# Kernel optimization log

Hardware: AMD Instinct MI355X
Metric: run time of the kernel (lower is better)

The kernel has to match this reference:

```python
import jax, jax.numpy as jnp
import numpy as np

B = 1; NCAM = 6; DM = 256; NH = 8; HD = 32; NL = 4; NP = 4; NZ = 2
BEV_H = 100; BEV_W = 100; NQ = BEV_H * BEV_W
IMG_H = 450; IMG_W = 800
SHAPES = [(56, 100), (28, 50), (14, 25), (7, 13)]
Z_CANDI = [0.0, 2.0]
H_METERS = 100.0; W_METERS = 100.0; OFFSET = 0.0
DFF = 1024


def _grid3d():
    # generate_grid + V_inv projection + z-anchor stacking (GenerateGrid)
    xs = (np.arange(BEV_W) + 0.5) / BEV_W
    ys = (np.arange(BEV_H) + 0.5) / BEV_H
    X, Y = np.meshgrid(xs, ys, indexing='xy')
    g = np.stack([X * BEV_W, Y * BEV_H, np.ones_like(X)], 0).reshape(3, -1)
    sh = BEV_H / H_METERS; sw = BEV_W / W_METERS
    V = np.array([[0., -sw, BEV_W / 2.], [-sh, 0., BEV_H * OFFSET + BEV_H / 2.], [0., 0., 1.]])
    g = np.linalg.inv(V) @ g  # (3, NQ), meters
    g3 = np.stack([np.concatenate([g[:2], np.full((1, g.shape[1]), z)], 0) for z in Z_CANDI], 0)
    return jnp.asarray(g3, jnp.float32)  # (NZ, 3, NQ)


def _ref2d():
    x = np.linspace(0, 1, BEV_W); y = np.linspace(0, 1, BEV_H)
    X, Y = np.meshgrid(x, y, indexing='xy')
    return jnp.asarray(np.stack([X, Y], -1).reshape(1, NQ, 2), jnp.float32)


def _pos_emb():
    # PositionEmbeddingSine(num_pos_feats=128, normalize=True)
    nf = DM // 2; scale = 2 * np.pi; eps = 1e-6
    y = (np.arange(1, BEV_H + 1, dtype=np.float64) - 0.5) / (BEV_H + eps) * scale
    x = (np.arange(1, BEV_W + 1, dtype=np.float64) - 0.5) / (BEV_W + eps) * scale
    dim_t = 10000.0 ** (2 * (np.arange(nf) // 2) / nf)
    def emb(v):
        p = v[:, None] / dim_t
        return np.stack([np.sin(p[:, 0::2]), np.cos(p[:, 1::2])], -1).reshape(v.shape[0], nf)
    ey = emb(y); ex = emb(x)
    pos = np.concatenate([np.broadcast_to(ey[:, None, :], (BEV_H, BEV_W, nf)),
                          np.broadcast_to(ex[None, :, :], (BEV_H, BEV_W, nf))], -1)
    return jnp.asarray(pos.reshape(1, NQ, DM), jnp.float32)


def _project(I, E):
    # ReferencePoints.get_3d
    g = _grid3d()
    g = jnp.concatenate([g, jnp.ones((NZ, 1, NQ), jnp.float32)], 1)  # (NZ,4,NQ) homo
    cam = jnp.einsum('bnij,djl->bndil', E, g)               # (B,N,NZ,4,NQ)
    img = jnp.einsum('bnij,bndjl->bndil', I, cam[:, :, :, :3])  # (B,N,NZ,3,NQ)
    eps = 1e-5
    z = img[:, :, :, 2:3]
    pts = img[:, :, :, :2] / jnp.maximum(z, eps)
    m = (z > eps) & (pts[:, :, :, 0:1] > 0) & (pts[:, :, :, 0:1] < IMG_W) \
        & (pts[:, :, :, 1:2] > 0) & (pts[:, :, :, 1:2] < IMG_H)
    pts = pts / jnp.array([IMG_W, IMG_H], jnp.float32)[None, None, None, :, None]
    ref = pts.transpose(0, 1, 4, 2, 3)                       # (B,N,NQ,NZ,2)
    mask = jnp.broadcast_to(m, (B, NCAM, NZ, 2, NQ)).transpose(0, 1, 4, 2, 3)
    return ref, mask


def _ln(x, g, b):
    mu = x.mean(-1, keepdims=True)
    var = ((x - mu) ** 2).mean(-1, keepdims=True)
    return (x - mu) * jax.lax.rsqrt(var + 1e-5) * g + b


def _bilinear(value, loc, H, W):
    # grid_sample, bilinear, zero padding, align_corners=False
    # value: (BB, H*W, C); loc: (BB, Q, 2) normalized (x,y) in [0,1]
    x = loc[..., 0] * W - 0.5
    y = loc[..., 1] * H - 0.5
    x0 = jnp.floor(x); y0 = jnp.floor(y)
    wx = (x - x0)[..., None]; wy = (y - y0)[..., None]
    x0 = x0.astype(jnp.int32); y0 = y0.astype(jnp.int32)
    def g(xi, yi):
        ok = ((xi >= 0) & (xi < W) & (yi >= 0) & (yi < H))[..., None]
        idx = jnp.clip(yi, 0, H - 1) * W + jnp.clip(xi, 0, W - 1)
        return jnp.take_along_axis(value, idx[..., None], axis=1) * ok
    return (g(x0, y0) * (1 - wx) * (1 - wy) + g(x0 + 1, y0) * wx * (1 - wy)
            + g(x0, y0 + 1) * (1 - wx) * wy + g(x0 + 1, y0 + 1) * wx * wy)


def _forward(queries_prev, features_0, features_1, features_2, features_3, intrinsics, extrinsic,
             bev_q_init, level_embed, cams_embed,
             ws_off, bs_off, ws_attn, bs_attn, ws_val, bs_val, ws_out, bs_out, g1, be1,
             wc_off, bc_off, wc_attn, bc_attn, wc_val, bc_val, wc_out, bc_out, g2, be2,
             w1, b1, w2, b2, g3, be3):
    feats = [features_0, features_1, features_2, features_3]
    queries = bev_q_init[None] + queries_prev  # (B,NQ,DM)
    ref3d, bmask = _project(intrinsics, extrinsic)
    ref2d = _ref2d(); pos = _pos_emb()
    # ---- deformable self-attention over the BEV grid (single level) ----
    q = queries + pos
    off = (q @ ws_off + bs_off).reshape(B, NQ, NH, NP, 2)
    aw = jax.nn.softmax((q @ ws_attn + bs_attn).reshape(B, NQ, NH, NP), -1)
    val = (queries @ ws_val + bs_val).reshape(B, NQ, NH, HD).transpose(0, 2, 1, 3).reshape(B * NH, NQ, HD)
    loc = ref2d[:, :, None, None, :] + off / jnp.array([BEV_W, BEV_H], jnp.float32)
    loc = loc.transpose(0, 2, 1, 3, 4).reshape(B * NH, NQ * NP, 2)
    s = _bilinear(val, loc, BEV_H, BEV_W).reshape(B, NH, NQ, NP, HD)
    sa = jnp.einsum('bhqpe,bqhp->bqhe', s, aw).reshape(B, NQ, DM) @ ws_out + bs_out
    queries = _ln(queries + sa, g1, be1)
    # ---- multi-camera multi-scale deformable cross-attention ----
    q = queries + pos
    offc = (q @ wc_off + bc_off).reshape(B, NQ, NH, NL, NZ, NP, 2)
    awc = jax.nn.softmax((q @ wc_attn + bc_attn).reshape(B, NQ, NH, NL * NZ * NP), -1)
    awc = awc.reshape(B, NQ, NH, NL, NZ, NP)
    acc = jnp.zeros((B, NCAM, NQ, NH, HD), queries.dtype)
    for l in range(NL):
        Hl, Wl = SHAPES[l]
        f = feats[l].reshape(B, NCAM, DM, Hl * Wl).transpose(0, 1, 3, 2)
        f = f + level_embed[l] + cams_embed[None, :, None, :]
        v = (f @ wc_val + bc_val).reshape(B, NCAM, Hl * Wl, NH, HD)
        v = v.transpose(0, 1, 3, 2, 4).reshape(B * NCAM * NH, Hl * Wl, HD)
        loc = ref3d[:, :, :, None, :, None, :] + (offc[:, None, :, :, l] / jnp.array([Wl, Hl], jnp.float32))
        loc = loc.transpose(0, 1, 3, 2, 4, 5, 6).reshape(B * NCAM * NH, NQ * NZ * NP, 2)
        s = _bilinear(v, loc, Hl, Wl).reshape(B, NCAM, NH, NQ, NZ, NP, HD)
        acc = acc + jnp.einsum('bnhqzpe,bqhzp->bnqhe', s, awc[:, :, :, l])
    out = acc.reshape(B, NCAM, NQ, DM) @ wc_out + bc_out
    valid = jnp.any(bmask[..., 0], axis=-1).astype(queries.dtype)  # (B,NCAM,NQ)
    cnt = jnp.maximum(valid.sum(1), 1.0)
    ca = (out * valid[..., None]).sum(1) / cnt[..., None]
    queries = _ln(queries + ca, g2, be2)
    # ---- FFN ----
    h = jax.nn.relu(queries @ w1 + b1) @ w2 + b2
    queries = _ln(queries + h, g3, be3)
    return queries


def setup_inputs() -> dict:
    key = jax.random.key(0)
    ks = jax.random.split(key, 24)
    def w(k, shape, s=0.02):
        return jax.random.normal(k, shape, jnp.float32) * s
    inp = {}
    inp['queries_prev'] = w(ks[0], (B, NQ, DM), 1.0)
    for i, (Hl, Wl) in enumerate(SHAPES):
        inp['features_' + str(i)] = w(ks[1 + i], (B * NCAM, DM, Hl, Wl), 1.0)
    I = np.zeros((B, NCAM, 3, 3), np.float32)
    I[..., 0, 0] = 400.0; I[..., 1, 1] = 400.0
    I[..., 0, 2] = IMG_W / 2.0; I[..., 1, 2] = IMG_H / 2.0; I[..., 2, 2] = 1.0
    Es = []
    for i in range(NCAM):
        th = 2 * np.pi * i / NCAM
        fwd = np.array([np.cos(th), np.sin(th), 0.0])
        rgt = np.array([np.sin(th), -np.cos(th), 0.0])
        dwn = np.array([0.0, 0.0, -1.0])
        R = np.stack([rgt, dwn, fwd], 0)
        t = -R @ (1.0 * fwd + np.array([0.0, 0.0, 1.5]))
        E = np.eye(4, dtype=np.float32); E[:3, :3] = R; E[:3, 3] = t
        Es.append(E)
    inp['intrinsics'] = jnp.asarray(I)
    inp['extrinsic'] = jnp.asarray(np.stack(Es).astype(np.float32)[None])
    inp['bev_q_init'] = w(ks[5], (NQ, DM))
    inp['level_embed'] = w(ks[6], (NL, DM))
    inp['cams_embed'] = w(ks[7], (NCAM, DM))
    inp['ws_off'] = w(ks[8], (DM, NH * NP * 2)); inp['bs_off'] = jnp.zeros((NH * NP * 2,), jnp.float32)
    inp['ws_attn'] = w(ks[9], (DM, NH * NP)); inp['bs_attn'] = jnp.zeros((NH * NP,), jnp.float32)
    inp['ws_val'] = w(ks[10], (DM, DM)); inp['bs_val'] = jnp.zeros((DM,), jnp.float32)
    inp['ws_out'] = w(ks[11], (DM, DM)); inp['bs_out'] = jnp.zeros((DM,), jnp.float32)
    inp['g1'] = jnp.ones((DM,), jnp.float32); inp['be1'] = jnp.zeros((DM,), jnp.float32)
    inp['wc_off'] = w(ks[12], (DM, NH * NL * NZ * NP * 2)); inp['bc_off'] = jnp.zeros((NH * NL * NZ * NP * 2,), jnp.float32)
    inp['wc_attn'] = w(ks[13], (DM, NH * NL * NZ * NP)); inp['bc_attn'] = jnp.zeros((NH * NL * NZ * NP,), jnp.float32)
    inp['wc_val'] = w(ks[14], (DM, DM)); inp['bc_val'] = jnp.zeros((DM,), jnp.float32)
    inp['wc_out'] = w(ks[15], (DM, DM)); inp['bc_out'] = jnp.zeros((DM,), jnp.float32)
    inp['g2'] = jnp.ones((DM,), jnp.float32); inp['be2'] = jnp.zeros((DM,), jnp.float32)
    inp['w1'] = w(ks[16], (DM, DFF)); inp['b1'] = jnp.zeros((DFF,), jnp.float32)
    inp['w2'] = w(ks[17], (DFF, DM)); inp['b2'] = jnp.zeros((DM,), jnp.float32)
    inp['g3'] = jnp.ones((DM,), jnp.float32); inp['be3'] = jnp.zeros((DM,), jnp.float32)
    return inp


def reference(queries_prev, features_0, features_1, features_2, features_3, intrinsics, extrinsic,
              bev_q_init, level_embed, cams_embed,
              ws_off, bs_off, ws_attn, bs_attn, ws_val, bs_val, ws_out, bs_out, g1, be1,
              wc_off, bc_off, wc_attn, bc_attn, wc_val, bc_val, wc_out, bc_out, g2, be2,
              w1, b1, w2, b2, g3, be3):
    return _forward(queries_prev, features_0, features_1, features_2, features_3, intrinsics, extrinsic,
                    bev_q_init, level_embed, cams_embed,
                    ws_off, bs_off, ws_attn, bs_attn, ws_val, bs_val, ws_out, bs_out, g1, be1,
                    wc_off, bc_off, wc_attn, bc_attn, wc_val, bc_val, wc_out, bc_out, g2, be2,
                    w1, b1, w2, b2, g3, be3)
```

## Files before the change

kernel.cpp:

```cpp
#include <hip/hip_runtime.h>
#include <hip/hip_bf16.h>
#include <math.h>

typedef __hip_bfloat16 bf16;
typedef __attribute__((ext_vector_type(8))) short short8;
typedef __attribute__((ext_vector_type(4))) float f32x4;
typedef __attribute__((ext_vector_type(2))) float f32x2;

__device__ __forceinline__ float b2f(bf16 v) { return __bfloat162float(v); }
__device__ __forceinline__ unsigned short f2bf(float f) {
    bf16 h = __float2bfloat16(f);
    return *(unsigned short*)&h;
}
__device__ __forceinline__ float bflo(unsigned u) { return __uint_as_float(u << 16); }
__device__ __forceinline__ float bfhi(unsigned u) { return __uint_as_float(u & 0xFFFF0000u); }
__device__ __forceinline__ f32x2 bf2(unsigned u) {
    f32x2 r;
    r.x = __uint_as_float(u << 16);
    r.y = __uint_as_float(u & 0xFFFF0000u);
    return r;
}

__device__ __forceinline__ float ldin(const void* p, size_t i, int isbf) {
    return isbf ? b2f(((const bf16*)p)[i]) : ((const float*)p)[i];
}

__global__ void detect_kernel(const unsigned* __restrict__ g1raw, int* __restrict__ flag)
{
    if (threadIdx.x == 0 && blockIdx.x == 0)
        flag[0] = (g1raw[0] == 0x3F803F80u) ? 1 : 0;
}

struct WTArg { const void* src[10]; int K[10]; int N[10]; int dstoff[10]; int cumt[11]; };
__global__ __launch_bounds__(256) void convert_wt_kernel(WTArg a, const int* __restrict__ flagp,
                                                         bf16* __restrict__ dst)
{
    __shared__ float T[64][65];
    int b = blockIdx.x, t = threadIdx.x;
    int isbf = flagp[0];
    int i = 0;
    while (b >= a.cumt[i + 1]) i++;
    int r = b - a.cumt[i];
    int K = a.K[i], N = a.N[i];
    int ntn = (N + 63) >> 6;
    int tk = r / ntn, tn = r - tk * ntn;
    int k0 = tk * 64, n0 = tn * 64;
    int nn = t & 63, kr = t >> 6;
#pragma unroll
    for (int ii = 0; ii < 16; ii++) {
        int k = kr + ii * 4;
        float v = 0.f;
        if (n0 + nn < N) v = ldin(a.src[i], (size_t)(k0 + k) * N + n0 + nn, isbf);
        T[k][nn] = v;
    }
    __syncthreads();
    int k2 = (t & 31) * 2, nr = t >> 5;
#pragma unroll
    for (int ii = 0; ii < 8; ii++) {
        int n = nr + ii * 8;
        if (n0 + n < N) {
            unsigned lo = f2bf(T[k2][n]);
            unsigned hi = f2bf(T[k2 + 1][n]);
            *(unsigned*)&dst[a.dstoff[i] + (size_t)(n0 + n) * K + k0 + k2] = lo | (hi << 16);
        }
    }
}

struct VConvArg { const void* src[16]; int cum[17]; };
__global__ __launch_bounds__(256) void convert_v_kernel(VConvArg a, const int* __restrict__ flagp,
                                                        float* __restrict__ dst)
{
    int g = blockIdx.x * 256 + threadIdx.x;
    if (g >= a.cum[16]) return;
    int isbf = flagp[0];
    int i = 0;
    while (g >= a.cum[i + 1]) i++;
    dst[g] = ldin(a.src[i], g - a.cum[i], isbf);
}

__global__ __launch_bounds__(256) void ptable_kernel(float* __restrict__ ptab)
{
    int idx = blockIdx.x * 256 + threadIdx.x;
    if (idx >= 12800) return;
    int a = idx >> 7, dd = idx & 127;
    float v = ((float)a + 0.5f) * (6.2831853071795864f / 100.000001f);
    float e = (float)(dd & ~1) * (1.f / 128.f);
    float freq = expf(e * 9.210340371976184f);
    float tt = v / freq;
    ptab[idx] = (dd & 1) ? cosf(tt) : sinf(tt);
}

#define KSTR 72
template<int BM>
__global__ __launch_bounds__(256) void mfma_gemm_t(
    const bf16* __restrict__ A, const bf16* __restrict__ Wt,
    const float* __restrict__ bias, float* __restrict__ C, bf16* __restrict__ Cbf,
    int M, int N, int K, int act)
{
    constexpr int MT = BM / 32;
    __shared__ unsigned short As[BM * KSTR];
    __shared__ unsigned short Ws[64 * KSTR];
    const int t = threadIdx.x;
    const int wave = t >> 6, lane = t & 63;
    const int qd = lane >> 4, l15 = lane & 15;
    const int m0 = blockIdx.x * BM, n0 = blockIdx.y * 64;
    const int wm = (wave >> 1) * (BM / 2), wn = (wave & 1) * 32;

    f32x4 acc[MT][2] = {};

    const int r_a = t >> 3, c8_a = t & 7;
    const int r_w = t >> 3, c8_w = t & 7;

    for (int k0 = 0; k0 < K; k0 += 64) {
        uint4 va[MT], vw[2];
#pragma unroll
        for (int i = 0; i < MT; i++)
            va[i] = *(const uint4*)(A + (size_t)(m0 + r_a + i * 32) * K + k0 + c8_a * 8);
#pragma unroll
        for (int i = 0; i < 2; i++)
            vw[i] = *(const uint4*)(Wt + (size_t)(n0 + r_w + i * 32) * K + k0 + c8_w * 8);
#pragma unroll
        for (int i = 0; i < MT; i++)
            *(uint4*)&As[(r_a + i * 32) * KSTR + c8_a * 8] = va[i];
#pragma unroll
        for (int i = 0; i < 2; i++)
            *(uint4*)&Ws[(r_w + i * 32) * KSTR + c8_w * 8] = vw[i];
        __syncthreads();
#pragma unroll
        for (int kk = 0; kk < 2; kk++) {
            short8 af[MT], bfr[2];
#pragma unroll
            for (int mi = 0; mi < MT; mi++)
                af[mi] = *(const short8*)&As[(wm + mi * 16 + l15) * KSTR + kk * 32 + qd * 8];
#pragma unroll
            for (int ni = 0; ni < 2; ni++)
                bfr[ni] = *(const short8*)&Ws[(wn + ni * 16 + l15) * KSTR + kk * 32 + qd * 8];
#pragma unroll
            for (int mi = 0; mi < MT; mi++)
#pragma unroll
                for (int ni = 0; ni < 2; ni++)
                    acc[mi][ni] = __builtin_amdgcn_mfma_f32_16x16x32_bf16(af[mi], bfr[ni], acc[mi][ni], 0, 0, 0);
        }
        __syncthreads();
    }
#pragma unroll
    for (int mi = 0; mi < MT; mi++) {
#pragma unroll
        for (int ni = 0; ni < 2; ni++) {
            int col = n0 + wn + ni * 16 + l15;
            if (col >= N) continue;
            float bv = bias ? bias[col] : 0.f;
#pragma unroll
            for (int r = 0; r < 4; r++) {
                int rowm = m0 + wm + mi * 16 + qd * 4 + r;
                if (rowm >= M) continue;
                float v = acc[mi][ni][r] + bv;
                if (act == 1) v = fmaxf(v, 0.f);
                if (Cbf) Cbf[(size_t)rowm * N + col] = __float2bfloat16(v);
                else     C[(size_t)rowm * N + col] = v;
            }
        }
    }
}

__global__ __launch_bounds__(256) void init_kernel(
    const void* __restrict__ qprev, const void* __restrict__ qinit, const int* __restrict__ flagp,
    const float* __restrict__ ptab,
    float* __restrict__ queries, bf16* __restrict__ queries_bf, bf16* __restrict__ qbuf_bf)
{
    int qi = blockIdx.x, d = threadIdx.x;
    int isbf = flagp[0];
    size_t idx = (size_t)qi * 256 + d;
    float qv = ldin(qinit, idx, isbf) + ldin(qprev, idx, isbf);
    int row = qi / 100, col = qi % 100;
    float pv = (d < 128) ? ptab[row * 128 + d] : ptab[col * 128 + (d - 128)];
    queries[idx] = qv;
    queries_bf[idx] = __float2bfloat16(qv);
    qbuf_bf[idx] = __float2bfloat16(qv + pv);
}

__global__ __launch_bounds__(256) void proj_kernel(
    const void* __restrict__ intr, const void* __restrict__ extr, const int* __restrict__ flagp,
    float* __restrict__ ref3d, float* __restrict__ valid)
{
    int idx = blockIdx.x * 256 + threadIdx.x;
    if (idx >= 60000) return;
    int isbf = flagp[0];
    int cam = idx / 10000, qi = idx % 10000;
    int row = qi / 100, col = qi % 100;
    float X = 49.5f - (float)row, Y = 49.5f - (float)col;
    float E[12];
#pragma unroll
    for (int i = 0; i < 12; i++) E[i] = ldin(extr, cam * 16 + i, isbf);
    float I9[9];
#pragma unroll
    for (int i = 0; i < 9; i++) I9[i] = ldin(intr, cam * 9 + i, isbf);
    bool any = false;
#pragma unroll
    for (int z = 0; z < 2; z++) {
        float Z = (z == 0) ? 0.f : 2.f;
        float c0 = E[0] * X + E[1] * Y + E[2] * Z + E[3];
        float c1 = E[4] * X + E[5] * Y + E[6] * Z + E[7];
        float c2 = E[8] * X + E[9] * Y + E[10] * Z + E[11];
        float i0 = I9[0] * c0 + I9[1] * c1 + I9[2] * c2;
        float i1 = I9[3] * c0 + I9[4] * c1 + I9[5] * c2;
        float i2 = I9[6] * c0 + I9[7] * c1 + I9[8] * c2;
        float zc = fmaxf(i2, 1e-5f);
        float px = i0 / zc, py = i1 / zc;
        bool m = (i2 > 1e-5f) && (px > 0.f) && (px < 800.f) && (py > 0.f) && (py < 450.f);
        any = any || m;
        ref3d[cam * 40000 + qi * 4 + z * 2 + 0] = px * (1.f / 800.f);
        ref3d[cam * 40000 + qi * 4 + z * 2 + 1] = py * (1.f / 450.f);
    }
    valid[cam * 10000 + qi] = any ? 1.f : 0.f;
}

__global__ __launch_bounds__(256) void tsa_sample_kernel(
    const float* __restrict__ ps, const float* __restrict__ val, bf16* __restrict__ sa_pre_bf)
{
    int blk = (blockIdx.x & 7) * 625 + (blockIdx.x >> 3);
    int qbase = blk * 2;
    int t = threadIdx.x;
    __shared__ float s_ps[192];
    __shared__ int4   s_tidx[64];
    __shared__ float4 s_tw[64];
    if (t < 192) s_ps[t] = ps[(size_t)qbase * 96 + t];
    __syncthreads();
    if (t < 64) {
        int q = t >> 5, r = t & 31, h = r >> 2, p = r & 3;
        int qi = qbase + q;
        const float* pq = s_ps + q * 96;
        float a0 = pq[64 + h * 4 + 0], a1 = pq[64 + h * 4 + 1];
        float a2 = pq[64 + h * 4 + 2], a3 = pq[64 + h * 4 + 3];
        float m = fmaxf(fmaxf(a0, a1), fmaxf(a2, a3));
        float den = expf(a0 - m) + expf(a1 - m) + expf(a2 - m) + expf(a3 - m);
        float aw = expf(pq[64 + h * 4 + p] - m) / den;
        float rx = (float)(qi % 100) * (1.f / 99.f);
        float ry = (float)(qi / 100) * (1.f / 99.f);
        float lx = rx + pq[h * 8 + p * 2 + 0] * 0.01f;
        float ly = ry + pq[h * 8 + p * 2 + 1] * 0.01f;
        float x = fminf(fmaxf(lx * 100.f - 0.5f, -2.0e6f), 2.0e6f);
        float y = fminf(fmaxf(ly * 100.f - 0.5f, -2.0e6f), 2.0e6f);
        float xf = floorf(x), yf = floorf(y);
        int x0 = (int)xf, y0 = (int)yf;
        float wx = x - xf, wy = y - yf;
        bool okx0 = (x0 >= 0) && (x0 < 100), okx1 = (x0 + 1 >= 0) && (x0 + 1 < 100);
        bool oky0 = (y0 >= 0) && (y0 < 100), oky1 = (y0 + 1 >= 0) && (y0 + 1 < 100);
        int x0c = min(max(x0, 0), 99), x1c = min(max(x0 + 1, 0), 99);
        int y0c = min(max(y0, 0), 99), y1c = min(max(y0 + 1, 0), 99);
        s_tidx[t] = make_int4((y0c * 100 + x0c) * 256, (y0c * 100 + x1c) * 256,
                              (y1c * 100 + x0c) * 256, (y1c * 100 + x1c) * 256);
        s_tw[t] = make_float4(aw * (1.f - wx) * (1.f - wy) * ((okx0 && oky0) ? 1.f : 0.f),
                              aw * wx * (1.f - wy) * ((okx1 && oky0) ? 1.f : 0.f),
                              aw * (1.f - wx) * wy * ((okx0 && oky1) ? 1.f : 0.f),
                              aw * wx * wy * ((okx1 && oky1) ? 1.f : 0.f));
    }
    __syncthreads();
    int q = t >> 7, c2 = t & 127, h = c2 >> 4;
    f32x2 V[4][4];
    float4 W[4];
#pragma unroll
    for (int p = 0; p < 4; p++) {
        int4 ix = s_tidx[q * 32 + h * 4 + p];
        W[p] = s_tw[q * 32 + h * 4 + p];
        V[p][0] = *(const f32x2*)(val + ix.x + 2 * c2);
        V[p][1] = *(const f32x2*)(val + ix.y + 2 * c2);
        V[p][2] = *(const f32x2*)(val + ix.z + 2 * c2);
        V[p][3] = *(const f32x2*)(val + ix.w + 2 * c2);
    }
    f32x2 acc = {0.f, 0.f};
#pragma unroll
    for (int p = 0; p < 4; p++)
        acc += V[p][0] * W[p].x + V[p][1] * W[p].y + V[p][2] * W[p].z + V[p][3] * W[p].w;
    int qi = qbase + q;
    unsigned lo = (unsigned)f2bf(acc.x) | ((unsigned)f2bf(acc.y) << 16);
    *(unsigned*)&sa_pre_bf[(size_t)qi * 256 + c2 * 2] = lo;
}

__global__ __launch_bounds__(256) void build_f_t_kernel(
    const void* __restrict__ f0, const void* __restrict__ f1,
    const void* __restrict__ f2, const void* __restrict__ f3,
    const void* __restrict__ lvl_emb, const void* __restrict__ cam_emb,
    const int* __restrict__ flagp, bf16* __restrict__ f_all)
{
    const int HWs[4]   = {5600, 1400, 350, 91};
    const int ptls[4]  = {88, 22, 6, 2};
    const int cumt[5]  = {0, 2112, 2640, 2784, 2832};
    const int rowb[4]  = {0, 33600, 42000, 44100};
    __shared__ float T[64][65];
    int b = blockIdx.x, t = threadIdx.x;
    int isbf = flagp[0];
    int l = 0;
    while (b >= cumt[l + 1]) l++;
    int r = b - cumt[l];
    int npt = ptls[l], HW = HWs[l];
    int cam = r / (4 * npt); r -= cam * 4 * npt;
    int dt = r / npt;
    int pt = r - dt * npt;
    const void* f = (l == 0) ? f0 : (l == 1) ? f1 : (l == 2) ? f2 : f3;

    int p = t & 63, dr = t >> 6;
    int pix = pt * 64 + p;
#pragma unroll
    for (int i = 0; i < 16; i++) {
        int d = dr + i * 4;
        float v = 0.f;
        if (pix < HW) v = ldin(f, (size_t)(cam * 256 + dt * 64 + d) * HW + pix, isbf);
        T[d][p] = v;
    }
    __syncthreads();
    int c2 = t & 31, pr0 = t >> 5;
    int dcol = dt * 64 + c2 * 2;
    float emb0 = ldin(lvl_emb, l * 256 + dcol, isbf) + ldin(cam_emb, cam * 256 + dcol, isbf);
    float emb1 = ldin(lvl_emb, l * 256 + dcol + 1, isbf) + ldin(cam_emb, cam * 256 + dcol + 1, isbf);
#pragma unroll
    for (int i = 0; i < 8; i++) {
        int px = pt * 64 + pr0 + i * 8;
        if (px < HW) {
            unsigned lo = f2bf(T[c2 * 2][pr0 + i * 8] + emb0);
            unsigned hi = f2bf(T[c2 * 2 + 1][pr0 + i * 8] + emb1);
            *(unsigned*)&f_all[(size_t)(rowb[l] + cam * HW + px) * 256 + dcol] = lo | (hi << 16);
        }
    }
}

__global__ __launch_bounds__(256) void cross_sample_kernel(
    const float* __restrict__ ref3d, const float* __restrict__ valid,
    const float* __restrict__ projc, const bf16* __restrict__ vall,
    bf16* __restrict__ ca_pre_bf, float* __restrict__ anyv)
{
    int qi = (blockIdx.x & 7) * 1250 + (blockIdx.x >> 3);
    int t = threadIdx.x;
    __shared__ float s_off[512];
    __shared__ float s_aw[256], s_ref[24], s_val[8];
    __shared__ int   s_cam[8];
    __shared__ int   s_nv;
    __shared__ int4   s_idx[512];
    __shared__ float4 s_w[512];
    const float* row = projc + (size_t)qi * 768;
    s_off[t]       = row[t];
    s_off[256 + t] = row[256 + t];
    float araw     = row[512 + t];
    if (t < 24) s_ref[t] = ref3d[(t >> 2) * 40000 + qi * 4 + (t & 3)];
    if (t >= 32 && t < 38) s_val[t - 32] = valid[(t - 32) * 10000 + qi];
    float m = araw;
#pragma unroll
    for (int mask = 16; mask >= 1; mask >>= 1) m = fmaxf(m, __shfl_xor(m, mask));
    float ev = expf(araw - m);
    float ssum = ev;
#pragma unroll
    for (int mask = 16; mask >= 1; mask >>= 1) ssum += __shfl_xor(ssum, mask);
    s_aw[t] = ev / ssum;
    __syncthreads();

    if (t == 0) {
        int n = 0;
#pragma unroll
        for (int c = 0; c < 6; c++)
            if (s_val[c] != 0.f) s_cam[n++] = c;
        s_nv = n;
    }
    __syncthreads();
    const int nv = s_nv;

    const int   Hs[4]    = {56, 28, 14, 7};
    const int   Wl[4]    = {100, 50, 25, 13};
    const int   HWs[4]   = {5600, 1400, 350, 91};
    const int   bases[4] = {0, 33600, 42000, 44100};
    const float invW[4]  = {1.f / 100.f, 1.f / 50.f, 1.f / 25.f, 1.f / 13.f};
    const float invH[4]  = {1.f / 56.f, 1.f / 28.f, 1.f / 14.f, 1.f / 7.f};

    const int c8 = t & 31, g = t >> 5, h = c8 >> 2;
    f32x2 q01 = {0.f, 0.f}, q23 = {0.f, 0.f}, q45 = {0.f, 0.f}, q67 = {0.f, 0.f};
    const unsigned short* vp = (const unsigned short*)vall;

    for (int cc0 = 0; cc0 < nv; cc0 += 2) {
#pragma unroll
        for (int cl = 0; cl < 2; cl++) {
            int e = t + cl * 256;
            if (cc0 + cl < nv) {
                int cam = s_cam[cc0 + cl];
                int rem = e & 255;
                int s = rem >> 3, hh = rem & 7;
                int l = s >> 3, z = (s >> 2) & 1;
                int W = Wl[l], H = Hs[l];
                float lx = s_ref[cam * 4 + z * 2 + 0] + s_off[hh * 64 + s * 2 + 0] * invW[l];
                float ly = s_ref[cam * 4 + z * 2 + 1] + s_off[hh * 64 + s * 2 + 1] * invH[l];
                float x = fminf(fmaxf(lx * (float)W - 0.5f, -2.0e6f), 2.0e6f);
                float y = fminf(fmaxf(ly * (float)H - 0.5f, -2.0e6f), 2.0e6f);
                float xf = floorf(x), yf = floorf(y);
                int x0 = (int)xf, y0 = (int)yf;
                float wx = x - xf, wy = y - yf;
                bool okx0 = (x0 >= 0) && (x0 < W);
                bool okx1 = (x0 + 1 >= 0) && (x0 + 1 < W);
                bool oky0 = (y0 >= 0) && (y0 < H);
                bool oky1 = (y0 + 1 >= 0) && (y0 + 1 < H);
                int x0c = min(max(x0, 0), W - 1), x1c = min(max(x0 + 1, 0), W - 1);
                int y0c = min(max(y0, 0), H - 1), y1c = min(max(y0 + 1, 0), H - 1);
                int base = (bases[l] + cam * HWs[l]) * 256;
                float awv = s_aw[hh * 32 + s];
                s_idx[e] = make_int4(base + (y0c * W + x0c) * 256,
                                     base + (y0c * W + x1c) * 256,
                                     base + (y1c * W + x0c) * 256,
                                     base + (y1c * W + x1c) * 256);
                s_w[e] = make_float4(awv * (1.f - wx) * (1.f - wy) * (okx0 && oky0 ? 1.f : 0.f),
                                     awv * wx * (1.f - wy) * (okx1 && oky0 ? 1.f : 0.f),
                                     awv * (1.f - wx) * wy * (okx0 && oky1 ? 1.f : 0.f),
                                     awv * wx * wy * (okx1 && oky1 ? 1.f : 0.f));
            }
        }
        __syncthreads();

#pragma unroll
        for (int cl = 0; cl < 2; cl++) {
            if (cc0 + cl < nv) {
                int eb = cl * 256 + g * 32 + h;
                int4   IX[4];
                float4 W[4];
                uint4  U[4][4];
#pragma unroll
                for (int j = 0; j < 4; j++) { IX[j] = s_idx[eb + j * 8]; W[j] = s_w[eb + j * 8]; }
#pragma unroll
                for (int j = 0; j < 4; j++) {
                    U[j][0] = *(const uint4*)(vp + IX[j].x + c8 * 8);
                    U[j][1] = *(const uint4*)(vp + IX[j].y + c8 * 8);
                    U[j][2] = *(const uint4*)(vp + IX[j].z + c8 * 8);
                    U[j][3] = *(const uint4*)(vp + IX[j].w + c8 * 8);
                }
#pragma unroll
                for (int j = 0; j < 4; j++) {
                    float4 w = W[j];
                    q01 += bf2(U[j][0].x) * w.x + bf2(U[j][1].x) * w.y + bf2(U[j][2].x) * w.z + bf2(U[j][3].x) * w.w;
                    q23 += bf2(U[j][0].y) * w.x + bf2(U[j][1].y) * w.y + bf2(U[j][2].y) * w.z + bf2(U[j][3].y) * w.w;
                    q45 += bf2(U[j][0].z) * w.x + bf2(U[j][1].z) * w.y + bf2(U[j][2].z) * w.z + bf2(U[j][3].z) * w.w;
                    q67 += bf2(U[j][0].w) * w.x + bf2(U[j][1].w) * w.y + bf2(U[j][2].w) * w.z + bf2(U[j][3].w) * w.w;
                }
            }
        }
        __syncthreads();
    }

    float inv_cnt = 1.f / fmaxf((float)nv, 1.f);
    float4* s_red = (float4*)s_idx;
    s_red[t]       = make_float4(q01.x, q01.y, q23.x, q23.y);
    s_red[256 + t] = make_float4(q45.x, q45.y, q67.x, q67.y);
    __syncthreads();
    if (t < 32) {
        float4 A = make_float4(0.f, 0.f, 0.f, 0.f), B = make_float4(0.f, 0.f, 0.f, 0.f);
#pragma unroll
        for (int gg = 0; gg < 8; gg++) {
            float4 a = s_red[gg * 32 + t], b = s_red[256 + gg * 32 + t];
            A.x += a.x; A.y += a.y; A.z += a.z; A.w += a.w;
            B.x += b.x; B.y += b.y; B.z += b.z; B.w += b.w;
        }
        unsigned w0 = (unsigned)f2bf(A.x * inv_cnt) | ((unsigned)f2bf(A.y * inv_cnt) << 16);
        unsigned w1 = (unsigned)f2bf(A.z * inv_cnt) | ((unsigned)f2bf(A.w * inv_cnt) << 16);
        unsigned w2 = (unsigned)f2bf(B.x * inv_cnt) | ((unsigned)f2bf(B.y * inv_cnt) << 16);
        unsigned w3 = (unsigned)f2bf(B.z * inv_cnt) | ((unsigned)f2bf(B.w * inv_cnt) << 16);
        *(uint4*)&ca_pre_bf[(size_t)qi * 256 + t * 8] = make_uint4(w0, w1, w2, w3);
    }
    if (t == 0) anyv[qi] = (nv > 0) ? 1.f : 0.f;
}

__global__ __launch_bounds__(256) void ln_kernel(
    float* __restrict__ queries, const float* __restrict__ x,
    const float* __restrict__ rowflag, const float* __restrict__ extra_bias,
    const float* __restrict__ g, const float* __restrict__ be,
    bf16* __restrict__ qpos_bf, bf16* __restrict__ nrm_bf, float* __restrict__ nrm_f32,
    const float* __restrict__ ptab)
{
    int qi = blockIdx.x, d = threadIdx.x;
    size_t idx = (size_t)qi * 256 + d;
    float r = queries[idx] + x[idx];
    if (extra_bias) r += rowflag[qi] * extra_bias[d];
    __shared__ float red1[4], red2[4];
    float s = r;
#pragma unroll
    for (int o = 32; o > 0; o >>= 1) s += __shfl_down(s, o, 64);
    if ((d & 63) == 0) red1[d >> 6] = s;
    __syncthreads();
    float mu = (red1[0] + red1[1] + red1[2] + red1[3]) * (1.f / 256.f);
    float dv = r - mu;
    float s2 = dv * dv;
#pragma unroll
    for (int o = 32; o > 0; o >>= 1) s2 += __shfl_down(s2, o, 64);
    if ((d & 63) == 0) red2[d >> 6] = s2;
    __syncthreads();
    float var = (red2[0] + red2[1] + red2[2] + red2[3]) * (1.f / 256.f);
    float nrm = dv * rsqrtf(var + 1e-5f) * g[d] + be[d];
    queries[idx] = nrm;
    if (qpos_bf) {
        int row = qi / 100, col = qi % 100;
        float pv = (d < 128) ? ptab[row * 128 + d] : ptab[col * 128 + (d - 128)];
        qpos_bf[idx] = __float2bfloat16(nrm + pv);
    }
    if (nrm_bf)  nrm_bf[idx]  = __float2bfloat16(nrm);
    if (nrm_f32) nrm_f32[idx] = nrm;
}

extern "C" void kernel_launch(void* const* d_in, const int* in_sizes, int n_in,
                              void* d_out, int out_size, void* d_ws, size_t ws_size,
                              hipStream_t stream)
{
    const void* qprev   = d_in[0];
    const void* f0      = d_in[1];
    const void* f1      = d_in[2];
    const void* f2      = d_in[3];
    const void* f3      = d_in[4];
    const void* intr    = d_in[5];
    const void* extr    = d_in[6];
    const void* qinit   = d_in[7];
    const void* lvl_emb = d_in[8];
    const void* cam_emb = d_in[9];

    float* ws = (float*)d_ws;
    float* queries    = ws + 0;
    float* ref3d      = ws + 2560000;
    float* valid      = ws + 2800000;
    float* anyv       = ws + 2860000;
    int*   flagp      = (int*)(ws + 2870000);
    float* biases     = ws + 2880000;
    bf16*  wconv_bf   = (bf16*)(ws + 2890000);
    bf16*  queries_bf = (bf16*)(ws + 3400000);
    bf16*  qbuf_bf    = (bf16*)(ws + 4680000);
    float* proj_s     = ws + 5960000;
    float* projc      = ws + 6920000;
    bf16*  vall_bf    = (bf16*)(ws + 14600000);
    float* RA         = ws + 20320000;
    float* val        = RA;
    bf16*  sa_pre_bf  = (bf16*)(RA + 2560000);
    float* sa         = RA + 3840000;
    bf16*  f_all_bf   = (bf16*)RA;
    bf16*  ca_pre_bf  = (bf16*)RA;
    float* ca         = RA + 1280000;
    bf16*  q2_bf      = (bf16*)(RA + 3840000);
    bf16*  hffn_bf    = (bf16*)(RA + 5120000);
    float* ffnout     = RA + 10240000;
    float* ptab       = ws + 33150000;

    if (ws_size < (size_t)33320000 * sizeof(float)) return;

    WTArg wa;
    {
        const int si[10] = {10, 12, 14, 16, 20, 22, 24, 26, 30, 32};
        const int Ks[10] = {256, 256, 256, 256, 256, 256, 256, 256, 256, 1024};
        const int Ns[10] = {64, 32, 256, 256, 512, 256, 256, 256, 1024, 256};
        int cum = 0, cumt = 0;
        for (int i = 0; i < 10; i++) {
            wa.src[i] = d_in[si[i]]; wa.K[i] = Ks[i]; wa.N[i] = Ns[i];
            wa.dstoff[i] = cum; wa.cumt[i] = cumt;
            cum += Ks[i] * Ns[i];
            cumt += ((Ks[i] + 63) / 64) * ((Ns[i] + 63) / 64);
        }
        wa.cumt[10] = cumt;
    }
    const bf16 *Wt_ws_fused = wconv_bf + 0;
    const bf16 *Wt_ws_val   = wconv_bf + 24576,  *Wt_ws_out = wconv_bf + 90112;
    const bf16 *Wt_wc_fused = wconv_bf + 155648;
    const bf16 *Wt_wc_val   = wconv_bf + 352256, *Wt_wc_out = wconv_bf + 417792;
    const bf16 *Wt_w1       = wconv_bf + 483328, *Wt_w2     = wconv_bf + 745472;

    VConvArg va;
    {
        const int si[16] = {11, 13, 15, 17, 18, 19, 21, 23, 25, 27, 28, 29, 31, 33, 34, 35};
        const int sz[16] = {64, 32, 256, 256, 256, 256, 512, 256, 256, 256, 256, 256, 1024, 256, 256, 256};
        int cum = 0;
        for (int i = 0; i < 16; i++) { va.src[i] = d_in[si[i]]; va.cum[i] = cum; cum += sz[i]; }
        va.cum[16] = cum;
    }
    const float *B_bs_fused = biases + 0;
    const float *B_bs_val = biases + 96,   *B_bs_out  = biases + 352;
    const float *B_g1     = biases + 608,  *B_be1     = biases + 864;
    const float *B_bc_fused = biases + 1120;
    const float *B_bc_val = biases + 1888, *B_bc_out  = biases + 2144;
    const float *B_g2     = biases + 2400, *B_be2     = biases + 2656;
    const float *B_b1     = biases + 2912, *B_b2      = biases + 3936;
    const float *B_g3     = biases + 4192, *B_be3     = biases + 4448;

    detect_kernel<<<1, 64, 0, stream>>>((const unsigned*)d_in[18], flagp);
    convert_wt_kernel<<<248, 256, 0, stream>>>(wa, flagp, wconv_bf);
    convert_v_kernel<<<(4704 + 255) / 256, 256, 0, stream>>>(va, flagp, biases);
    ptable_kernel<<<50, 256, 0, stream>>>(ptab);
    init_kernel<<<10000, 256, 0, stream>>>(qprev, qinit, flagp, ptab, queries, queries_bf, qbuf_bf);
    proj_kernel<<<(60000 + 255) / 256, 256, 0, stream>>>(intr, extr, flagp, ref3d, valid);
    mfma_gemm_t<64><<<dim3(157, 2), 256, 0, stream>>>(qbuf_bf, Wt_ws_fused, B_bs_fused, proj_s, nullptr, 10000, 96, 256, 0);
    mfma_gemm_t<64><<<dim3(157, 4), 256, 0, stream>>>(queries_bf, Wt_ws_val, B_bs_val, val, nullptr, 10000, 256, 256, 0);
    tsa_sample_kernel<<<5000, 256, 0, stream>>>(proj_s, val, sa_pre_bf);
    mfma_gemm_t<64><<<dim3(157, 4), 256, 0, stream>>>(sa_pre_bf, Wt_ws_out, B_bs_out, sa, nullptr, 10000, 256, 256, 0);
    ln_kernel<<<10000, 256, 0, stream>>>(queries, sa, nullptr, nullptr, B_g1, B_be1, qbuf_bf, nullptr, nullptr, ptab);
    mfma_gemm_t<128><<<dim3(79, 12), 256, 0, stream>>>(qbuf_bf, Wt_wc_fused, B_bc_fused, projc, nullptr, 10000, 768, 256, 0);
    build_f_t_kernel<<<2832, 256, 0, stream>>>(f0, f1, f2, f3, lvl_emb, cam_emb, flagp, f_all_bf);
    mfma_gemm_t<128><<<dim3(349, 4), 256, 0, stream>>>(f_all_bf, Wt_wc_val, B_bc_val, nullptr, vall_bf, 44646, 256, 256, 0);
    cross_sample_kernel<<<10000, 256, 0, stream>>>(ref3d, valid, projc, vall_bf, ca_pre_bf, anyv);
    mfma_gemm_t<64><<<dim3(157, 4), 256, 0, stream>>>(ca_pre_bf, Wt_wc_out, nullptr, ca, nullptr, 10000, 256, 256, 0);
    ln_kernel<<<10000, 256, 0, stream>>>(queries, ca, anyv, B_bc_out, B_g2, B_be2, nullptr, q2_bf, nullptr, ptab);
    mfma_gemm_t<128><<<dim3(79, 16), 256, 0, stream>>>(q2_bf, Wt_w1, B_b1, nullptr, hffn_bf, 10000, 1024, 256, 1);
    mfma_gemm_t<64><<<dim3(157, 4), 256, 0, stream>>>(hffn_bf, Wt_w2, B_b2, ffnout, nullptr, 10000, 256, 1024, 0);
    ln_kernel<<<10000, 256, 0, stream>>>(queries, ffnout, nullptr, nullptr, B_g3, B_be3, nullptr, nullptr, (float*)d_out, ptab);
}
```

Measured before the change: 460.3 us.

## Prefetch next GEMM K-tile, merge setup kernels, use 128-row GEMM tiles

The GEMM now loads the next K-tile from global memory into registers while the current tile's MFMAs run, a register-level double buffer. The dtype-detect kernel is removed: each kernel checks the g1 bit pattern inline. The bias conversion and sin/cos table kernels are merged into one launch. Several 10000x256 GEMMs move from 64-row to 128-row tiles, which halves the grid to 316 blocks and raises register pressure.

```diff
diff --git a/kernel.cpp b/kernel.cpp
--- a/kernel.cpp
+++ b/kernel.cpp
@@ -24,20 +24,17 @@
 __device__ __forceinline__ float ldin(const void* p, size_t i, int isbf) {
     return isbf ? b2f(((const bf16*)p)[i]) : ((const float*)p)[i];
 }
-
-__global__ void detect_kernel(const unsigned* __restrict__ g1raw, int* __restrict__ flag)
-{
-    if (threadIdx.x == 0 && blockIdx.x == 0)
-        flag[0] = (g1raw[0] == 0x3F803F80u) ? 1 : 0;
+__device__ __forceinline__ int sniff(const unsigned* g1raw) {
+    return (g1raw[0] == 0x3F803F80u) ? 1 : 0;
 }
 
 struct WTArg { const void* src[10]; int K[10]; int N[10]; int dstoff[10]; int cumt[11]; };
-__global__ __launch_bounds__(256) void convert_wt_kernel(WTArg a, const int* __restrict__ flagp,
+__global__ __launch_bounds__(256) void convert_wt_kernel(WTArg a, const unsigned* __restrict__ g1raw,
                                                          bf16* __restrict__ dst)
 {
     __shared__ float T[64][65];
     int b = blockIdx.x, t = threadIdx.x;
-    int isbf = flagp[0];
+    int isbf = sniff(g1raw);
     int i = 0;
     while (b >= a.cumt[i + 1]) i++;
     int r = b - a.cumt[i];
@@ -67,23 +64,21 @@
 }
 
 struct VConvArg { const void* src[16]; int cum[17]; };
-__global__ __launch_bounds__(256) void convert_v_kernel(VConvArg a, const int* __restrict__ flagp,
-                                                        float* __restrict__ dst)
+__global__ __launch_bounds__(256) void setup_kernel(VConvArg a, const unsigned* __restrict__ g1raw,
+                                                    float* __restrict__ dst, float* __restrict__ ptab)
 {
     int g = blockIdx.x * 256 + threadIdx.x;
-    if (g >= a.cum[16]) return;
-    int isbf = flagp[0];
-    int i = 0;
-    while (g >= a.cum[i + 1]) i++;
-    dst[g] = ldin(a.src[i], g - a.cum[i], isbf);
-}
-
-__global__ __launch_bounds__(256) void ptable_kernel(float* __restrict__ ptab)
-{
-    int idx = blockIdx.x * 256 + threadIdx.x;
+    if (g < a.cum[16]) {
+        int isbf = sniff(g1raw);
+        int i = 0;
+        while (g >= a.cum[i + 1]) i++;
+        dst[g] = ldin(a.src[i], g - a.cum[i], isbf);
+        return;
+    }
+    int idx = g - a.cum[16];
     if (idx >= 12800) return;
-    int a = idx >> 7, dd = idx & 127;
-    float v = ((float)a + 0.5f) * (6.2831853071795864f / 100.000001f);
+    int aa = idx >> 7, dd = idx & 127;
+    float v = ((float)aa + 0.5f) * (6.2831853071795864f / 100.000001f);
     float e = (float)(dd & ~1) * (1.f / 128.f);
     float freq = expf(e * 9.210340371976184f);
     float tt = v / freq;
@@ -111,14 +106,15 @@
     const int r_a = t >> 3, c8_a = t & 7;
     const int r_w = t >> 3, c8_w = t & 7;
 
+    uint4 va[MT], vw[2];
+#pragma unroll
+    for (int i = 0; i < MT; i++)
+        va[i] = *(const uint4*)(A + (size_t)(m0 + r_a + i * 32) * K + c8_a * 8);
+#pragma unroll
+    for (int i = 0; i < 2; i++)
+        vw[i] = *(const uint4*)(Wt + (size_t)(n0 + r_w + i * 32) * K + c8_w * 8);
+
     for (int k0 = 0; k0 < K; k0 += 64) {
-        uint4 va[MT], vw[2];
-#pragma unroll
-        for (int i = 0; i < MT; i++)
-            va[i] = *(const uint4*)(A + (size_t)(m0 + r_a + i * 32) * K + k0 + c8_a * 8);
-#pragma unroll
-        for (int i = 0; i < 2; i++)
-            vw[i] = *(const uint4*)(Wt + (size_t)(n0 + r_w + i * 32) * K + k0 + c8_w * 8);
 #pragma unroll
         for (int i = 0; i < MT; i++)
             *(uint4*)&As[(r_a + i * 32) * KSTR + c8_a * 8] = va[i];
@@ -126,6 +122,15 @@
         for (int i = 0; i < 2; i++)
             *(uint4*)&Ws[(r_w + i * 32) * KSTR + c8_w * 8] = vw[i];
         __syncthreads();
+        if (k0 + 64 < K) {
+            const int k1 = k0 + 64;
+#pragma unroll
+            for (int i = 0; i < MT; i++)
+                va[i] = *(const uint4*)(A + (size_t)(m0 + r_a + i * 32) * K + k1 + c8_a * 8);
+#pragma unroll
+            for (int i = 0; i < 2; i++)
+                vw[i] = *(const uint4*)(Wt + (size_t)(n0 + r_w + i * 32) * K + k1 + c8_w * 8);
+        }
 #pragma unroll
         for (int kk = 0; kk < 2; kk++) {
             short8 af[MT], bfr[2];
@@ -164,12 +169,12 @@
 }
 
 __global__ __launch_bounds__(256) void init_kernel(
-    const void* __restrict__ qprev, const void* __restrict__ qinit, const int* __restrict__ flagp,
+    const void* __restrict__ qprev, const void* __restrict__ qinit, const unsigned* __restrict__ g1raw,
     const float* __restrict__ ptab,
     float* __restrict__ queries, bf16* __restrict__ queries_bf, bf16* __restrict__ qbuf_bf)
 {
     int qi = blockIdx.x, d = threadIdx.x;
-    int isbf = flagp[0];
+    int isbf = sniff(g1raw);
     size_t idx = (size_t)qi * 256 + d;
     float qv = ldin(qinit, idx, isbf) + ldin(qprev, idx, isbf);
     int row = qi / 100, col = qi % 100;
@@ -180,12 +185,12 @@
 }
 
 __global__ __launch_bounds__(256) void proj_kernel(
-    const void* __restrict__ intr, const void* __restrict__ extr, const int* __restrict__ flagp,
+    const void* __restrict__ intr, const void* __restrict__ extr, const unsigned* __restrict__ g1raw,
     float* __restrict__ ref3d, float* __restrict__ valid)
 {
     int idx = blockIdx.x * 256 + threadIdx.x;
     if (idx >= 60000) return;
-    int isbf = flagp[0];
+    int isbf = sniff(g1raw);
     int cam = idx / 10000, qi = idx % 10000;
     int row = qi / 100, col = qi % 100;
     float X = 49.5f - (float)row, Y = 49.5f - (float)col;
@@ -281,7 +286,7 @@
     const void* __restrict__ f0, const void* __restrict__ f1,
     const void* __restrict__ f2, const void* __restrict__ f3,
     const void* __restrict__ lvl_emb, const void* __restrict__ cam_emb,
-    const int* __restrict__ flagp, bf16* __restrict__ f_all)
+    const unsigned* __restrict__ g1raw, bf16* __restrict__ f_all)
 {
     const int HWs[4]   = {5600, 1400, 350, 91};
     const int ptls[4]  = {88, 22, 6, 2};
@@ -289,7 +294,7 @@
     const int rowb[4]  = {0, 33600, 42000, 44100};
     __shared__ float T[64][65];
     int b = blockIdx.x, t = threadIdx.x;
-    int isbf = flagp[0];
+    int isbf = sniff(g1raw);
     int l = 0;
     while (b >= cumt[l + 1]) l++;
     int r = b - cumt[l];
@@ -512,13 +517,13 @@
     const void* qinit   = d_in[7];
     const void* lvl_emb = d_in[8];
     const void* cam_emb = d_in[9];
+    const unsigned* g1raw = (const unsigned*)d_in[18];
 
     float* ws = (float*)d_ws;
     float* queries    = ws + 0;
     float* ref3d      = ws + 2560000;
     float* valid      = ws + 2800000;
     float* anyv       = ws + 2860000;
-    int*   flagp      = (int*)(ws + 2870000);
     float* biases     = ws + 2880000;
     bf16*  wconv_bf   = (bf16*)(ws + 2890000);
     bf16*  queries_bf = (bf16*)(ws + 3400000);
@@ -577,24 +582,22 @@
     const float *B_b1     = biases + 2912, *B_b2      = biases + 3936;
     const float *B_g3     = biases + 4192, *B_be3     = biases + 4448;
 
-    detect_kernel<<<1, 64, 0, stream>>>((const unsigned*)d_in[18], flagp);
-    convert_wt_kernel<<<248, 256, 0, stream>>>(wa, flagp, wconv_bf);
-    convert_v_kernel<<<(4704 + 255) / 256, 256, 0, stream>>>(va, flagp, biases);
-    ptable_kernel<<<50, 256, 0, stream>>>(ptab);
-    init_kernel<<<10000, 256, 0, stream>>>(qprev, qinit, flagp, ptab, queries, queries_bf, qbuf_bf);
-    proj_kernel<<<(60000 + 255) / 256, 256, 0, stream>>>(intr, extr, flagp, ref3d, valid);
-    mfma_gemm_t<64><<<dim3(157, 2), 256, 0, stream>>>(qbuf_bf, Wt_ws_fused, B_bs_fused, proj_s, nullptr, 10000, 96, 256, 0);
-    mfma_gemm_t<64><<<dim3(157, 4), 256, 0, stream>>>(queries_bf, Wt_ws_val, B_bs_val, val, nullptr, 10000, 256, 256, 0);
+    convert_wt_kernel<<<248, 256, 0, stream>>>(wa, g1raw, wconv_bf);
+    setup_kernel<<<(4704 + 12800 + 255) / 256, 256, 0, stream>>>(va, g1raw, biases, ptab);
+    init_kernel<<<10000, 256, 0, stream>>>(qprev, qinit, g1raw, ptab, queries, queries_bf, qbuf_bf);
+    proj_kernel<<<(60000 + 255) / 256, 256, 0, stream>>>(intr, extr, g1raw, ref3d, valid);
+    mfma_gemm_t<128><<<dim3(79, 2), 256, 0, stream>>>(qbuf_bf, Wt_ws_fused, B_bs_fused, proj_s, nullptr, 10000, 96, 256, 0);
+    mfma_gemm_t<128><<<dim3(79, 4), 256, 0, stream>>>(queries_bf, Wt_ws_val, B_bs_val, val, nullptr, 10000, 256, 256, 0);
     tsa_sample_kernel<<<5000, 256, 0, stream>>>(proj_s, val, sa_pre_bf);
-    mfma_gemm_t<64><<<dim3(157, 4), 256, 0, stream>>>(sa_pre_bf, Wt_ws_out, B_bs_out, sa, nullptr, 10000, 256, 256, 0);
+    mfma_gemm_t<128><<<dim3(79, 4), 256, 0, stream>>>(sa_pre_bf, Wt_ws_out, B_bs_out, sa, nullptr, 10000, 256, 256, 0);
     ln_kernel<<<10000, 256, 0, stream>>>(queries, sa, nullptr, nullptr, B_g1, B_be1, qbuf_bf, nullptr, nullptr, ptab);
     mfma_gemm_t<128><<<dim3(79, 12), 256, 0, stream>>>(qbuf_bf, Wt_wc_fused, B_bc_fused, projc, nullptr, 10000, 768, 256, 0);
-    build_f_t_kernel<<<2832, 256, 0, stream>>>(f0, f1, f2, f3, lvl_emb, cam_emb, flagp, f_all_bf);
+    build_f_t_kernel<<<2832, 256, 0, stream>>>(f0, f1, f2, f3, lvl_emb, cam_emb, g1raw, f_all_bf);
     mfma_gemm_t<128><<<dim3(349, 4), 256, 0, stream>>>(f_all_bf, Wt_wc_val, B_bc_val, nullptr, vall_bf, 44646, 256, 256, 0);
     cross_sample_kernel<<<10000, 256, 0, stream>>>(ref3d, valid, projc, vall_bf, ca_pre_bf, anyv);
-    mfma_gemm_t<64><<<dim3(157, 4), 256, 0, stream>>>(ca_pre_bf, Wt_wc_out, nullptr, ca, nullptr, 10000, 256, 256, 0);
+    mfma_gemm_t<128><<<dim3(79, 4), 256, 0, stream>>>(ca_pre_bf, Wt_wc_out, nullptr, ca, nullptr, 10000, 256, 256, 0);
     ln_kernel<<<10000, 256, 0, stream>>>(queries, ca, anyv, B_bc_out, B_g2, B_be2, nullptr, q2_bf, nullptr, ptab);
     mfma_gemm_t<128><<<dim3(79, 16), 256, 0, stream>>>(q2_bf, Wt_w1, B_b1, nullptr, hffn_bf, 10000, 1024, 256, 1);
-    mfma_gemm_t<64><<<dim3(157, 4), 256, 0, stream>>>(hffn_bf, Wt_w2, B_b2, ffnout, nullptr, 10000, 256, 1024, 0);
+    mfma_gemm_t<128><<<dim3(79, 4), 256, 0, stream>>>(hffn_bf, Wt_w2, B_b2, ffnout, nullptr, 10000, 256, 1024, 0);
     ln_kernel<<<10000, 256, 0, stream>>>(queries, ffnout, nullptr, nullptr, B_g3, B_be3, nullptr, nullptr, (float*)d_out, ptab);
 }
```

New measurement: 631.3 us. 37.2% more time.
